# Optimization experiments

Measured on AMD Instinct MI355X. Metric: run time of the kernel, lower is better.

## Reference

```python
import jax, jax.numpy as jnp
import numpy as np

B, N, D, E, C = 8, 4096, 1024, 512, 4096


def setup_inputs() -> dict:
    key = jax.random.key(0)
    k1, k2, k3 = jax.random.split(key, 3)
    x = jax.random.normal(k1, (B, N, D), dtype=jnp.float32)
    # xavier_normal_ scale for an (input_dim, codebook_dim) matrix
    scale = (2.0 / (D + E)) ** 0.5
    random_projection = jax.random.normal(k2, (D, E), dtype=jnp.float32) * scale
    codebook = jax.random.normal(k3, (C, E), dtype=jnp.float32)
    return {"x": x, "random_projection": random_projection, "codebook": codebook}


def _l2norm(v, eps=1e-12):
    # matches torch.nn.functional.normalize(p=2): v / max(||v||, eps)
    return v / jnp.maximum(jnp.linalg.norm(v, axis=-1, keepdims=True), eps)


def reference(x, random_projection, codebook):
    # project: b n d, d e -> b n e
    proj = jnp.einsum("bnd,de->bne", x, random_projection)
    pn = _l2norm(proj)            # [B, N, E], unit vectors
    cn = _l2norm(codebook)        # [C, E],   unit vectors
    # For unit vectors, ||p - c||^2 = 2 - 2 * <p, c>, so
    # argmin_c cdist == argmax_c cosine similarity (same indices as torch code).
    sim = jnp.einsum("bne,ce->bnc", pn, cn)  # [B, N, C]
    xq = jnp.argmax(sim, axis=-1).astype(jnp.int32)  # [B, N]
    return xq
```

## Files before the change

### kernel.cpp

```cpp
#include <hip/hip_runtime.h>
#include <math.h>


typedef _Float16 half8 __attribute__((ext_vector_type(8)));
typedef _Float16 half4 __attribute__((ext_vector_type(4)));
typedef float f32x4 __attribute__((ext_vector_type(4)));

#define INV2048 (4.8828125e-4f)
#define MARGIN 0.03f

struct Split { _Float16 h, l; };

__device__ __forceinline__ Split split_f32(float v) {
    Split s;
    s.h = (_Float16)v;
    s.l = (_Float16)((v - (float)s.h) * 2048.0f);
    return s;
}

__device__ __forceinline__ void gl_lds16(const void* g, void* l) {
    __builtin_amdgcn_global_load_lds(
        (const __attribute__((address_space(1))) unsigned int*)g,
        (__attribute__((address_space(3))) unsigned int*)l, 16, 0, 0);
}

__global__ __launch_bounds__(256) void k_prep_rpt(const float* __restrict__ rp,
                                                  _Float16* __restrict__ th,
                                                  _Float16* __restrict__ tl,
                                                  int* __restrict__ cnt) {
    if (blockIdx.x == 0 && blockIdx.y == 0 && threadIdx.x == 0) *cnt = 0;
    __shared__ float tile[64][65];
    const int k0 = blockIdx.x * 64, n0 = blockIdx.y * 64;
    const int t = threadIdx.x;
    const int rr = t >> 6, cc = t & 63;
    #pragma unroll
    for (int i = 0; i < 16; ++i) {
        int r = i * 4 + rr;
        tile[r][cc] = rp[(size_t)(k0 + r) * 512 + n0 + cc];
    }
    __syncthreads();
    #pragma unroll
    for (int i = 0; i < 16; ++i) {
        int n = i * 4 + rr;
        Split s = split_f32(tile[cc][n]);
        size_t o = (size_t)(n0 + n) * 1024 + k0 + cc;
        th[o] = s.h;
        tl[o] = s.l;
    }
}

__global__ __launch_bounds__(256) void k_norm_cb(const float* __restrict__ cb,
                                                 _Float16* __restrict__ ch,
                                                 _Float16* __restrict__ cl) {
    const int c = blockIdx.x;
    const int t = threadIdx.x;
    const float* row = cb + (size_t)c * 512;
    float v0 = row[t];
    float v1 = row[t + 256];
    float ss = v0 * v0 + v1 * v1;
    #pragma unroll
    for (int o = 32; o > 0; o >>= 1) ss += __shfl_down(ss, o, 64);
    __shared__ float wsum[4];
    if ((t & 63) == 0) wsum[t >> 6] = ss;
    __syncthreads();
    float s = 1.0f / fmaxf(sqrtf(wsum[0] + wsum[1] + wsum[2] + wsum[3]), 1e-12f);
    Split s0 = split_f32(v0 * s);
    ch[(size_t)c * 512 + t] = s0.h;
    cl[(size_t)c * 512 + t] = s0.l;
    Split s1 = split_f32(v1 * s);
    ch[(size_t)c * 512 + t + 256] = s1.h;
    cl[(size_t)c * 512 + t + 256] = s1.l;
}

__global__ __launch_bounds__(256, 2) void k_gemm1(const float* __restrict__ X,
                                                  const _Float16* __restrict__ Bh,
                                                  const _Float16* __restrict__ Bl,
                                                  _Float16* __restrict__ Ph,
                                                  _Float16* __restrict__ Pl) {
    __shared__ _Float16 sAh[128 * 32], sAl[128 * 32], sBh[128 * 32], sBl[128 * 32];
    const int t = threadIdx.x;
    const int nb = blockIdx.x;
    const int mb = blockIdx.y;
    const int lane = t & 63, w = t >> 6;
    const int quad = lane >> 4, l15 = lane & 15;
    const int wm = w >> 1, wn = w & 1;

    f32x4 acc[4][4], acc2[4][4];
    const f32x4 z = {0.f, 0.f, 0.f, 0.f};
    #pragma unroll
    for (int i = 0; i < 4; ++i)
        #pragma unroll
        for (int j = 0; j < 4; ++j) { acc[i][j] = z; acc2[i][j] = z; }

    const int srow = w * 32 + (lane >> 2);
    const int kcol = (lane & 3) * 8;
    const _Float16* gBh = Bh + (size_t)(nb * 128 + srow) * 1024 + kcol;
    const _Float16* gBl = Bl + (size_t)(nb * 128 + srow) * 1024 + kcol;
    const float* Xb = X + (size_t)(mb * 128) * 1024;

    for (int ks = 0; ks < 32; ++ks) {
        const int ko = ks * 32;
        __syncthreads();
        gl_lds16(gBh + ko, &sBh[w * 1024]);
        gl_lds16(gBh + ko + (size_t)16 * 1024, &sBh[w * 1024 + 512]);
        gl_lds16(gBl + ko, &sBl[w * 1024]);
        gl_lds16(gBl + ko + (size_t)16 * 1024, &sBl[w * 1024 + 512]);
        #pragma unroll
        for (int i = 0; i < 4; ++i) {
            int c = i * 256 + t;
            int row = c >> 3, kq = (c & 7) * 4;
            float4 v = *(const float4*)(Xb + (size_t)row * 1024 + ko + kq);
            Split sx = split_f32(v.x), sy = split_f32(v.y);
            Split sz = split_f32(v.z), sw = split_f32(v.w);
            half4 hv, lv;
            hv.x = sx.h; hv.y = sy.h; hv.z = sz.h; hv.w = sw.h;
            lv.x = sx.l; lv.y = sy.l; lv.z = sz.l; lv.w = sw.l;
            *(half4*)&sAh[row * 32 + kq] = hv;
            *(half4*)&sAl[row * 32 + kq] = lv;
        }
        __syncthreads();
        half8 ah[4], al[4], bh[4], bl[4];
        #pragma unroll
        for (int i = 0; i < 4; ++i) {
            ah[i] = *(const half8*)&sAh[(wm * 64 + i * 16 + l15) * 32 + quad * 8];
            al[i] = *(const half8*)&sAl[(wm * 64 + i * 16 + l15) * 32 + quad * 8];
            bh[i] = *(const half8*)&sBh[(wn * 64 + i * 16 + l15) * 32 + quad * 8];
            bl[i] = *(const half8*)&sBl[(wn * 64 + i * 16 + l15) * 32 + quad * 8];
        }
        #pragma unroll
        for (int mi = 0; mi < 4; ++mi)
            #pragma unroll
            for (int ni = 0; ni < 4; ++ni) {
                acc[mi][ni]  = __builtin_amdgcn_mfma_f32_16x16x32_f16(ah[mi], bh[ni], acc[mi][ni], 0, 0, 0);
                acc2[mi][ni] = __builtin_amdgcn_mfma_f32_16x16x32_f16(ah[mi], bl[ni], acc2[mi][ni], 0, 0, 0);
                acc2[mi][ni] = __builtin_amdgcn_mfma_f32_16x16x32_f16(al[mi], bh[ni], acc2[mi][ni], 0, 0, 0);
            }
    }
    #pragma unroll
    for (int mi = 0; mi < 4; ++mi)
        #pragma unroll
        for (int r = 0; r < 4; ++r) {
            int row = mb * 128 + wm * 64 + mi * 16 + quad * 4 + r;
            #pragma unroll
            for (int ni = 0; ni < 4; ++ni) {
                int col = nb * 128 + wn * 64 + ni * 16 + l15;
                float v = acc[mi][ni][r] + acc2[mi][ni][r] * INV2048;
                Split s = split_f32(v);
                Ph[(size_t)row * 512 + col] = s.h;
                Pl[(size_t)row * 512 + col] = s.l;
            }
        }
}

__global__ __launch_bounds__(256, 4) void k_sim_h(const _Float16* __restrict__ Ah,
                                                  const _Float16* __restrict__ Bh,
                                                  float* __restrict__ pv1,
                                                  int* __restrict__ pi1,
                                                  float* __restrict__ pv2) {
    __shared__ _Float16 sAh[128 * 32], sBh[128 * 32];
    __shared__ float v1s[128][2], v2s[128][2];
    __shared__ int   i1s[128][2];
    const int t = threadIdx.x;
    const int cbk = blockIdx.x;
    const int mb = blockIdx.y;
    const int lane = t & 63, w = t >> 6;
    const int quad = lane >> 4, l15 = lane & 15;
    const int wm = w >> 1, wn = w & 1;

    f32x4 acc[4][4];
    const f32x4 z = {0.f, 0.f, 0.f, 0.f};
    #pragma unroll
    for (int i = 0; i < 4; ++i)
        #pragma unroll
        for (int j = 0; j < 4; ++j) acc[i][j] = z;

    const int srow = w * 32 + (lane >> 2);
    const int kcol = (lane & 3) * 8;
    const _Float16* gAh = Ah + (size_t)(mb * 128 + srow) * 512 + kcol;
    const _Float16* gBh = Bh + (size_t)(cbk * 128 + srow) * 512 + kcol;

    for (int ks = 0; ks < 16; ++ks) {
        const int ko = ks * 32;
        __syncthreads();
        gl_lds16(gAh + ko, &sAh[w * 1024]);
        gl_lds16(gAh + ko + (size_t)16 * 512, &sAh[w * 1024 + 512]);
        gl_lds16(gBh + ko, &sBh[w * 1024]);
        gl_lds16(gBh + ko + (size_t)16 * 512, &sBh[w * 1024 + 512]);
        __syncthreads();
        half8 ah[4], bh[4];
        #pragma unroll
        for (int i = 0; i < 4; ++i) {
            ah[i] = *(const half8*)&sAh[(wm * 64 + i * 16 + l15) * 32 + quad * 8];
            bh[i] = *(const half8*)&sBh[(wn * 64 + i * 16 + l15) * 32 + quad * 8];
        }
        #pragma unroll
        for (int mi = 0; mi < 4; ++mi)
            #pragma unroll
            for (int ni = 0; ni < 4; ++ni)
                acc[mi][ni] = __builtin_amdgcn_mfma_f32_16x16x32_f16(ah[mi], bh[ni], acc[mi][ni], 0, 0, 0);
    }

    #pragma unroll
    for (int mi = 0; mi < 4; ++mi)
        #pragma unroll
        for (int r = 0; r < 4; ++r) {
            float v1 = -INFINITY, v2 = -INFINITY;
            int i1 = 0x7fffffff;
            #pragma unroll
            for (int ni = 0; ni < 4; ++ni) {
                float v = acc[mi][ni][r];
                int col = cbk * 128 + wn * 64 + ni * 16 + l15;
                if (v > v1 || (v == v1 && col < i1)) { v2 = v1; v1 = v; i1 = col; }
                else if (v > v2) v2 = v;
            }
            #pragma unroll
            for (int o = 1; o < 16; o <<= 1) {
                float ov1 = __shfl_xor(v1, o, 64);
                int oi1 = __shfl_xor(i1, o, 64);
                float ov2 = __shfl_xor(v2, o, 64);
                if (ov1 > v1 || (ov1 == v1 && oi1 < i1)) { v2 = fmaxf(v1, ov2); v1 = ov1; i1 = oi1; }
                else v2 = fmaxf(v2, ov1);
            }
            if (l15 == 0) {
                int row = wm * 64 + mi * 16 + quad * 4 + r;
                v1s[row][wn] = v1; i1s[row][wn] = i1; v2s[row][wn] = v2;
            }
        }
    __syncthreads();
    if (t < 128) {
        float v1 = v1s[t][0], v2 = v2s[t][0];
        int i1 = i1s[t][0];
        float ov1 = v1s[t][1], ov2 = v2s[t][1];
        int oi1 = i1s[t][1];
        if (ov1 > v1 || (ov1 == v1 && oi1 < i1)) { v2 = fmaxf(v1, ov2); v1 = ov1; i1 = oi1; }
        else v2 = fmaxf(v2, ov1);
        size_t o = (size_t)(mb * 128 + t) * 32 + cbk;
        pv1[o] = v1; pi1[o] = i1; pv2[o] = v2;
    }
}

__global__ __launch_bounds__(256) void k_flag(const float* __restrict__ pv1,
                                              const int* __restrict__ pi1,
                                              const float* __restrict__ pv2,
                                              int* __restrict__ out,
                                              int* __restrict__ list,
                                              int* __restrict__ cnt) {
    int r = blockIdx.x * 256 + threadIdx.x;
    if (r >= 32768) return;
    size_t base = (size_t)r * 32;
    float v1 = pv1[base], v2 = pv2[base];
    int i1 = pi1[base];
    #pragma unroll
    for (int j = 1; j < 32; ++j) {
        float ov1 = pv1[base + j], ov2 = pv2[base + j];
        int oi1 = pi1[base + j];
        if (ov1 > v1 || (ov1 == v1 && oi1 < i1)) { v2 = fmaxf(v1, ov2); v1 = ov1; i1 = oi1; }
        else v2 = fmaxf(v2, ov1);
    }
    out[r] = i1;
    if (v1 - v2 < MARGIN) {
        int p = atomicAdd(cnt, 1);
        list[p] = r;
    }
}

__global__ __launch_bounds__(256, 2) void k_sim_fix(const _Float16* __restrict__ Ah,
                                                    const _Float16* __restrict__ Al,
                                                    const _Float16* __restrict__ Bh,
                                                    const _Float16* __restrict__ Bl,
                                                    const int* __restrict__ list,
                                                    const int* __restrict__ cnt,
                                                    float* __restrict__ rpv,
                                                    int* __restrict__ rpi) {
    __shared__ _Float16 sAh[128 * 32], sAl[128 * 32], sBh[128 * 32], sBl[128 * 32];
    __shared__ int rowidx[128];
    __shared__ float pvs[128][2];
    __shared__ int   pis[128][2];
    const int count = *cnt;
    const int t = threadIdx.x;
    const int cbk = blockIdx.x;
    const int lane = t & 63, w = t >> 6;
    const int quad = lane >> 4, l15 = lane & 15;
    const int wm = w >> 1, wn = w & 1;

    const int srow = w * 32 + (lane >> 2);
    const int kcol = (lane & 3) * 8;
    const _Float16* gBh = Bh + (size_t)(cbk * 128 + srow) * 512 + kcol;
    const _Float16* gBl = Bl + (size_t)(cbk * 128 + srow) * 512 + kcol;

    for (int g = blockIdx.y; g * 128 < count; g += gridDim.y) {
        __syncthreads();
        if (t < 128) {
            int p = g * 128 + t;
            rowidx[t] = (p < count) ? list[p] : list[0];
        }
        __syncthreads();

        f32x4 acc[4][4], acc2[4][4];
        const f32x4 z = {0.f, 0.f, 0.f, 0.f};
        #pragma unroll
        for (int i = 0; i < 4; ++i)
            #pragma unroll
            for (int j = 0; j < 4; ++j) { acc[i][j] = z; acc2[i][j] = z; }

        for (int ks = 0; ks < 16; ++ks) {
            const int ko = ks * 32;
            __syncthreads();
            gl_lds16(gBh + ko, &sBh[w * 1024]);
            gl_lds16(gBh + ko + (size_t)16 * 512, &sBh[w * 1024 + 512]);
            gl_lds16(gBl + ko, &sBl[w * 1024]);
            gl_lds16(gBl + ko + (size_t)16 * 512, &sBl[w * 1024 + 512]);
            #pragma unroll
            for (int i = 0; i < 2; ++i) {
                int idx = i * 256 + t;
                int row = idx >> 2, seg = (idx & 3) * 8;
                size_t src = (size_t)rowidx[row] * 512 + ko + seg;
                *(half8*)&sAh[row * 32 + seg] = *(const half8*)(Ah + src);
                *(half8*)&sAl[row * 32 + seg] = *(const half8*)(Al + src);
            }
            __syncthreads();
            half8 ah[4], al[4], bh[4], bl[4];
            #pragma unroll
            for (int i = 0; i < 4; ++i) {
                ah[i] = *(const half8*)&sAh[(wm * 64 + i * 16 + l15) * 32 + quad * 8];
                al[i] = *(const half8*)&sAl[(wm * 64 + i * 16 + l15) * 32 + quad * 8];
                bh[i] = *(const half8*)&sBh[(wn * 64 + i * 16 + l15) * 32 + quad * 8];
                bl[i] = *(const half8*)&sBl[(wn * 64 + i * 16 + l15) * 32 + quad * 8];
            }
            #pragma unroll
            for (int mi = 0; mi < 4; ++mi)
                #pragma unroll
                for (int ni = 0; ni < 4; ++ni) {
                    acc[mi][ni]  = __builtin_amdgcn_mfma_f32_16x16x32_f16(ah[mi], bh[ni], acc[mi][ni], 0, 0, 0);
                    acc2[mi][ni] = __builtin_amdgcn_mfma_f32_16x16x32_f16(ah[mi], bl[ni], acc2[mi][ni], 0, 0, 0);
                    acc2[mi][ni] = __builtin_amdgcn_mfma_f32_16x16x32_f16(al[mi], bh[ni], acc2[mi][ni], 0, 0, 0);
                }
        }

        #pragma unroll
        for (int mi = 0; mi < 4; ++mi)
            #pragma unroll
            for (int r = 0; r < 4; ++r) {
                float bv = -INFINITY;
                int bi = 0x7fffffff;
                #pragma unroll
                for (int ni = 0; ni < 4; ++ni) {
                    float v = acc[mi][ni][r] + acc2[mi][ni][r] * INV2048;
                    int col = cbk * 128 + wn * 64 + ni * 16 + l15;
                    if (v > bv || (v == bv && col < bi)) { bv = v; bi = col; }
                }
                #pragma unroll
                for (int o = 1; o < 16; o <<= 1) {
                    float ov = __shfl_xor(bv, o, 64);
                    int oi = __shfl_xor(bi, o, 64);
                    if (ov > bv || (ov == bv && oi < bi)) { bv = ov; bi = oi; }
                }
                if (l15 == 0) {
                    int row = wm * 64 + mi * 16 + quad * 4 + r;
                    pvs[row][wn] = bv; pis[row][wn] = bi;
                }
            }
        __syncthreads();
        if (t < 128 && g * 128 + t < count) {
            float v0 = pvs[t][0], v1 = pvs[t][1];
            int i0 = pis[t][0], i1 = pis[t][1];
            bool sw = (v1 > v0) || (v1 == v0 && i1 < i0);
            size_t o = (size_t)(g * 128 + t) * 32 + cbk;
            rpv[o] = sw ? v1 : v0;
            rpi[o] = sw ? i1 : i0;
        }
    }
}

__global__ __launch_bounds__(256) void k_fix(const float* __restrict__ rpv,
                                             const int* __restrict__ rpi,
                                             const int* __restrict__ list,
                                             const int* __restrict__ cnt,
                                             int* __restrict__ out) {
    int p = blockIdx.x * 256 + threadIdx.x;
    if (p >= *cnt) return;
    size_t base = (size_t)p * 32;
    float bv = -INFINITY;
    int bi = 0x7fffffff;
    #pragma unroll
    for (int j = 0; j < 32; ++j) {
        float v = rpv[base + j];
        int ci = rpi[base + j];
        if (v > bv || (v == bv && ci < bi)) { bv = v; bi = ci; }
    }
    out[list[p]] = bi;
}

extern "C" void kernel_launch(void* const* d_in, const int* in_sizes, int n_in,
                              void* d_out, int out_size, void* d_ws, size_t ws_size,
                              hipStream_t stream) {
    const float* x  = (const float*)d_in[0];
    const float* rp = (const float*)d_in[1];
    const float* cb = (const float*)d_in[2];
    int* out = (int*)d_out;

    char* ws = (char*)d_ws;
    _Float16* cn_h   = (_Float16*)(ws);
    _Float16* cn_l   = (_Float16*)(ws + ((size_t)4 << 20));
    _Float16* rpT_h  = (_Float16*)(ws + ((size_t)8 << 20));
    _Float16* rpT_l  = (_Float16*)(ws + ((size_t)9 << 20));
    _Float16* proj_h = (_Float16*)(ws + ((size_t)10 << 20));
    _Float16* proj_l = (_Float16*)(ws + ((size_t)42 << 20));
    float*    pv1    = (float*)   (ws + ((size_t)74 << 20));
    int*      pi1    = (int*)     (ws + ((size_t)78 << 20));
    float*    pv2    = (float*)   (ws + ((size_t)82 << 20));
    float*    rpv    = (float*)   (ws + ((size_t)86 << 20));
    int*      rpi    = (int*)     (ws + ((size_t)90 << 20));
    int*      list   = (int*)     (ws + ((size_t)94 << 20));
    int*      cnt    = (int*)     (ws + ((size_t)94 << 20) + (128 << 10));

    k_prep_rpt<<<dim3(16, 8), 256, 0, stream>>>(rp, rpT_h, rpT_l, cnt);
    k_norm_cb<<<4096, 256, 0, stream>>>(cb, cn_h, cn_l);
    k_gemm1<<<dim3(4, 256), 256, 0, stream>>>(x, rpT_h, rpT_l, proj_h, proj_l);
    k_sim_h<<<dim3(32, 256), 256, 0, stream>>>(proj_h, cn_h, pv1, pi1, pv2);
    k_flag<<<128, 256, 0, stream>>>(pv1, pi1, pv2, out, list, cnt);
    k_sim_fix<<<dim3(32, 32), 256, 0, stream>>>(proj_h, proj_l, cn_h, cn_l, list, cnt, rpv, rpi);
    k_fix<<<128, 256, 0, stream>>>(rpv, rpi, list, cnt, out);
}
```

Before: 599.0 us.

## Load sim GEMM operands directly from global into registers with double buffering

The similarity GEMM kernel no longer stages A and B tiles through LDS with barriers. Each wave now loads its MFMA fragments straight from global memory into registers, using a two-stage register double buffer so the next K slice loads while the current one computes. Launch bounds drop from 4 to 3 waves per SIMD to make room for the extra registers. This removes the LDS traffic and syncthreads, but loses operand sharing between waves, so global and L2 traffic goes up and occupancy goes down.

Measured after the change: 940.4 us. +57.0%, slower.

```diff
diff --git a/kernel.cpp b/kernel.cpp
--- a/kernel.cpp
+++ b/kernel.cpp
@@ -152,12 +152,11 @@
         }
 }
 
-__global__ __launch_bounds__(256, 4) void k_sim_h(const _Float16* __restrict__ Ah,
+__global__ __launch_bounds__(256, 3) void k_sim_h(const _Float16* __restrict__ Ah,
                                                   const _Float16* __restrict__ Bh,
                                                   float* __restrict__ pv1,
                                                   int* __restrict__ pi1,
                                                   float* __restrict__ pv2) {
-    __shared__ _Float16 sAh[128 * 32], sBh[128 * 32];
     __shared__ float v1s[128][2], v2s[128][2];
     __shared__ int   i1s[128][2];
     const int t = threadIdx.x;
@@ -174,30 +173,38 @@
         #pragma unroll
         for (int j = 0; j < 4; ++j) acc[i][j] = z;
 
-    const int srow = w * 32 + (lane >> 2);
-    const int kcol = (lane & 3) * 8;
-    const _Float16* gAh = Ah + (size_t)(mb * 128 + srow) * 512 + kcol;
-    const _Float16* gBh = Bh + (size_t)(cbk * 128 + srow) * 512 + kcol;
-
-    for (int ks = 0; ks < 16; ++ks) {
-        const int ko = ks * 32;
-        __syncthreads();
-        gl_lds16(gAh + ko, &sAh[w * 1024]);
-        gl_lds16(gAh + ko + (size_t)16 * 512, &sAh[w * 1024 + 512]);
-        gl_lds16(gBh + ko, &sBh[w * 1024]);
-        gl_lds16(gBh + ko + (size_t)16 * 512, &sBh[w * 1024 + 512]);
-        __syncthreads();
-        half8 ah[4], bh[4];
+    const _Float16* aB = Ah + (size_t)(mb * 128 + wm * 64 + l15) * 512 + quad * 8;
+    const _Float16* bB = Bh + (size_t)(cbk * 128 + wn * 64 + l15) * 512 + quad * 8;
+
+    half8 a0[4], b0[4], a1[4], b1[4];
+    #pragma unroll
+    for (int i = 0; i < 4; ++i) {
+        a0[i] = *(const half8*)(aB + (size_t)i * 16 * 512);
+        b0[i] = *(const half8*)(bB + (size_t)i * 16 * 512);
+    }
+    for (int ks = 0; ks < 16; ks += 2) {
         #pragma unroll
         for (int i = 0; i < 4; ++i) {
-            ah[i] = *(const half8*)&sAh[(wm * 64 + i * 16 + l15) * 32 + quad * 8];
-            bh[i] = *(const half8*)&sBh[(wn * 64 + i * 16 + l15) * 32 + quad * 8];
+            a1[i] = *(const half8*)(aB + (size_t)i * 16 * 512 + (ks + 1) * 32);
+            b1[i] = *(const half8*)(bB + (size_t)i * 16 * 512 + (ks + 1) * 32);
         }
         #pragma unroll
         for (int mi = 0; mi < 4; ++mi)
             #pragma unroll
             for (int ni = 0; ni < 4; ++ni)
-                acc[mi][ni] = __builtin_amdgcn_mfma_f32_16x16x32_f16(ah[mi], bh[ni], acc[mi][ni], 0, 0, 0);
+                acc[mi][ni] = __builtin_amdgcn_mfma_f32_16x16x32_f16(a0[mi], b0[ni], acc[mi][ni], 0, 0, 0);
+        if (ks + 2 < 16) {
+            #pragma unroll
+            for (int i = 0; i < 4; ++i) {
+                a0[i] = *(const half8*)(aB + (size_t)i * 16 * 512 + (ks + 2) * 32);
+                b0[i] = *(const half8*)(bB + (size_t)i * 16 * 512 + (ks + 2) * 32);
+            }
+        }
+        #pragma unroll
+        for (int mi = 0; mi < 4; ++mi)
+            #pragma unroll
+            for (int ni = 0; ni < 4; ++ni)
+                acc[mi][ni] = __builtin_amdgcn_mfma_f32_16x16x32_f16(a1[mi], b1[ni], acc[mi][ni], 0, 0, 0);
     }
 
     #pragma unroll
```

## Double-buffer LDS tiles and XOR-swizzle layout in fp16 similarity GEMM

Applied to the files above, without the earlier changes.

The similarity kernel now keeps two LDS buffers for the A and B tiles. It issues the global-to-LDS loads for the next K step before running MFMAs on the current one, which removes one barrier per iteration and overlaps loads with compute. It also XOR-swizzles the 16-byte segments within each LDS row, on both the store and the read side, to cut bank conflicts on the half8 fragment reads. The cost is twice the LDS for tiles, which may reduce occupancy at the declared 4 blocks per CU.

Result: no change. 609.3 us (+1.7%).

```diff
diff --git a/kernel.cpp b/kernel.cpp
--- a/kernel.cpp
+++ b/kernel.cpp
@@ -157,7 +157,7 @@
                                                   float* __restrict__ pv1,
                                                   int* __restrict__ pi1,
                                                   float* __restrict__ pv2) {
-    __shared__ _Float16 sAh[128 * 32], sBh[128 * 32];
+    __shared__ _Float16 sA[2][4096], sB[2][4096];
     __shared__ float v1s[128][2], v2s[128][2];
     __shared__ int   i1s[128][2];
     const int t = threadIdx.x;
@@ -174,30 +174,39 @@
         #pragma unroll
         for (int j = 0; j < 4; ++j) acc[i][j] = z;
 
-    const int srow = w * 32 + (lane >> 2);
-    const int kcol = (lane & 3) * 8;
-    const _Float16* gAh = Ah + (size_t)(mb * 128 + srow) * 512 + kcol;
-    const _Float16* gBh = Bh + (size_t)(cbk * 128 + srow) * 512 + kcol;
+    const int srow = lane >> 2;
+    const int kseg = (lane & 3) ^ ((lane >> 3) & 3);
+    const _Float16* gA = Ah + (size_t)(mb * 128 + w * 32 + srow) * 512 + kseg * 8;
+    const _Float16* gB = Bh + (size_t)(cbk * 128 + w * 32 + srow) * 512 + kseg * 8;
+
+    const int sw8 = (quad ^ ((l15 >> 1) & 3)) * 8;
+
+    gl_lds16(gA, &sA[0][w * 1024]);
+    gl_lds16(gA + (size_t)16 * 512, &sA[0][w * 1024 + 512]);
+    gl_lds16(gB, &sB[0][w * 1024]);
+    gl_lds16(gB + (size_t)16 * 512, &sB[0][w * 1024 + 512]);
 
     for (int ks = 0; ks < 16; ++ks) {
-        const int ko = ks * 32;
-        __syncthreads();
-        gl_lds16(gAh + ko, &sAh[w * 1024]);
-        gl_lds16(gAh + ko + (size_t)16 * 512, &sAh[w * 1024 + 512]);
-        gl_lds16(gBh + ko, &sBh[w * 1024]);
-        gl_lds16(gBh + ko + (size_t)16 * 512, &sBh[w * 1024 + 512]);
-        __syncthreads();
-        half8 ah[4], bh[4];
+        const int p = ks & 1;
+        __syncthreads();
+        if (ks + 1 < 16) {
+            const int ko = (ks + 1) * 32;
+            gl_lds16(gA + ko, &sA[p ^ 1][w * 1024]);
+            gl_lds16(gA + ko + (size_t)16 * 512, &sA[p ^ 1][w * 1024 + 512]);
+            gl_lds16(gB + ko, &sB[p ^ 1][w * 1024]);
+            gl_lds16(gB + ko + (size_t)16 * 512, &sB[p ^ 1][w * 1024 + 512]);
+        }
+        half8 a[4], b[4];
         #pragma unroll
         for (int i = 0; i < 4; ++i) {
-            ah[i] = *(const half8*)&sAh[(wm * 64 + i * 16 + l15) * 32 + quad * 8];
-            bh[i] = *(const half8*)&sBh[(wn * 64 + i * 16 + l15) * 32 + quad * 8];
+            a[i] = *(const half8*)&sA[p][(wm * 64 + i * 16 + l15) * 32 + sw8];
+            b[i] = *(const half8*)&sB[p][(wn * 64 + i * 16 + l15) * 32 + sw8];
         }
         #pragma unroll
         for (int mi = 0; mi < 4; ++mi)
             #pragma unroll
             for (int ni = 0; ni < 4; ++ni)
-                acc[mi][ni] = __builtin_amdgcn_mfma_f32_16x16x32_f16(ah[mi], bh[ni], acc[mi][ni], 0, 0, 0);
+                acc[mi][ni] = __builtin_amdgcn_mfma_f32_16x16x32_f16(a[mi], b[ni], acc[mi][ni], 0, 0, 0);
     }
 
     #pragma unroll
```
